# Performance work log

Hardware: AMD Instinct MI355X
Metric: run time of the kernel (lower is better)

Reference implementation:

```python
import jax, jax.numpy as jnp
import numpy as np

HEADS = 8
DIM_HEAD = 64
DIM = 512
EPS = 1e-7  # module's self.eps, also used as LayerNorm eps


def _per_head_layernorm(t, w, b):
    # t: [b, h, n, d]; w, b: [h, d] (one LayerNorm per head, affine)
    mu = t.mean(axis=-1, keepdims=True)
    var = t.var(axis=-1, keepdims=True)  # biased, matches torch LayerNorm
    tn = (t - mu) * jax.lax.rsqrt(var + EPS)
    return tn * w[None, :, None, :] + b[None, :, None, :]


def setup_inputs() -> dict:
    key = jax.random.key(0)
    ks = jax.random.split(key, 4)
    inner = HEADS * DIM_HEAD
    return {
        "x": jax.random.normal(ks[0], (2, 2048, DIM), dtype=jnp.float32),
        "w_qkv": jax.random.normal(ks[1], (3 * inner, DIM), dtype=jnp.float32) * 0.02,
        "lnk_w": jnp.ones((HEADS, DIM_HEAD), dtype=jnp.float32),
        "lnk_b": jnp.zeros((HEADS, DIM_HEAD), dtype=jnp.float32),
        "lnv_w": jnp.ones((HEADS, DIM_HEAD), dtype=jnp.float32),
        "lnv_b": jnp.zeros((HEADS, DIM_HEAD), dtype=jnp.float32),
        "w_out": jax.random.normal(ks[2], (DIM, inner), dtype=jnp.float32) * 0.02,
        "b_out": jnp.zeros((DIM,), dtype=jnp.float32),
    }


def reference(x, w_qkv, lnk_w, lnk_b, lnv_w, lnv_b, w_out, b_out):
    b, n, _ = x.shape
    qkv = x @ w_qkv.T  # [b, n, 3*inner]
    q, k, v = jnp.split(qkv, 3, axis=-1)

    def split_heads(t):  # [b, n, h*d] -> [b, h, n, d]
        return t.reshape(b, n, HEADS, DIM_HEAD).transpose(0, 2, 1, 3)

    q, k, v = map(split_heads, (q, k, v))

    # per-head LayerNorm over dim_head on k and v
    k = _per_head_layernorm(k, lnk_w, lnk_b)
    v = _per_head_layernorm(v, lnv_w, lnv_b)

    # causal linear attention: prefix sums of k and of k-v outer products
    k_cum = jnp.cumsum(k, axis=2)  # [b, h, n, d]
    # scores: [b, h, n, d, e] prefix sums of outer products, scaled by 1/seq_len
    scores = jnp.cumsum(jnp.einsum('bhnd,bhne->bhnde', k, v), axis=2) / n
    d_inv = 1.0 / jnp.einsum('bhnd,bhnd->bhn', k_cum + EPS, q)  # [b, h, n]
    out = jnp.einsum('bhnd,bhnde,bhn->bhne', q, scores, d_inv)  # [b, h, n, e]

    out = out.transpose(0, 2, 1, 3).reshape(b, n, HEADS * DIM_HEAD)  # b n (h e)
    return out @ w_out.T + b_out
```

## Files before the change

### kernel.cpp

```cpp
#include <hip/hip_runtime.h>

constexpr int Bb   = 2;
constexpr int Nn   = 2048;
constexpr int Hh   = 8;
constexpr int Dd   = 64;
constexpr int Mm   = Bb * Nn;
constexpr int TQKV = 1536;
constexpr int INNER = Hh * Dd;
constexpr int CH   = 64;
constexpr int NCH  = Nn / CH;
constexpr int CSZ  = Dd * Dd + Dd;
constexpr float EPSF = 1e-7f;

typedef _Float16 half8 __attribute__((ext_vector_type(8)));
typedef _Float16 half4 __attribute__((ext_vector_type(4)));
typedef float f32x4 __attribute__((ext_vector_type(4)));

#define AS1(p) ((const __attribute__((address_space(1))) unsigned int*)(p))
#define AS3(p) ((__attribute__((address_space(3))) unsigned int*)(p))

__global__ __launch_bounds__(256) void gemm1_f32(
    const float* __restrict__ A, const float* __restrict__ B,
    float* __restrict__ C,
    const float* __restrict__ lnk_w, const float* __restrict__ lnk_b) {
  __shared__ float pool[8704];
  __shared__ float mean_s[128], inv_s[128];
  float* As = pool;
  float* Bs = pool + 4224;
  const int tid = threadIdx.x;
  const int tx = tid & 15, ty = tid >> 4;
  const int bm = blockIdx.y * 128, bn = blockIdx.x * 64;
  const int rowA = tid & 127, c4a = tid >> 7;
  const int rowB = tid & 63,  c4b = tid >> 6;

  float acc[8][4] = {};

  for (int k0 = 0; k0 < 512; k0 += 32) {
#pragma unroll
    for (int p = 0; p < 4; ++p) {
      int c4 = c4a + 2 * p;
      float4 fa = *(const float4*)(A + (size_t)(bm + rowA) * 512 + k0 + c4 * 4);
      As[(c4 * 4 + 0) * 132 + rowA] = fa.x; As[(c4 * 4 + 1) * 132 + rowA] = fa.y;
      As[(c4 * 4 + 2) * 132 + rowA] = fa.z; As[(c4 * 4 + 3) * 132 + rowA] = fa.w;
    }
#pragma unroll
    for (int p = 0; p < 2; ++p) {
      int c4 = c4b + 4 * p;
      float4 fb = *(const float4*)(B + (size_t)(bn + rowB) * 512 + k0 + c4 * 4);
      Bs[(c4 * 4 + 0) * 68 + rowB] = fb.x; Bs[(c4 * 4 + 1) * 68 + rowB] = fb.y;
      Bs[(c4 * 4 + 2) * 68 + rowB] = fb.z; Bs[(c4 * 4 + 3) * 68 + rowB] = fb.w;
    }
    __syncthreads();
#pragma unroll
    for (int kk = 0; kk < 32; ++kk) {
      float a[8], b[4];
      *(float4*)&a[0] = *(const float4*)&As[kk * 132 + ty * 8];
      *(float4*)&a[4] = *(const float4*)&As[kk * 132 + ty * 8 + 4];
      *(float4*)&b[0] = *(const float4*)&Bs[kk * 68 + tx * 4];
#pragma unroll
      for (int i = 0; i < 8; ++i)
#pragma unroll
        for (int j = 0; j < 4; ++j) acc[i][j] += a[i] * b[j];
    }
    __syncthreads();
  }

  if (bn < 512) {
#pragma unroll
    for (int i = 0; i < 8; ++i) {
      size_t row = bm + ty * 8 + i;
      float4 r;
      r.x = acc[i][0]; r.y = acc[i][1]; r.z = acc[i][2]; r.w = acc[i][3];
      *(float4*)(C + row * (size_t)TQKV + bn + tx * 4) = r;
    }
  } else {
#pragma unroll
    for (int i = 0; i < 8; ++i)
#pragma unroll
      for (int j = 0; j < 4; ++j)
        pool[(ty * 8 + i) * 68 + tx * 4 + j] = acc[i][j];
    __syncthreads();
    if (tid < 128) {
      const float* R = pool + tid * 68;
      float s = 0.f, s2 = 0.f;
#pragma unroll
      for (int j = 0; j < 64; j += 4) {
        float4 v = *(const float4*)&R[j];
        s += v.x + v.y + v.z + v.w;
        s2 += v.x * v.x + v.y * v.y + v.z * v.z + v.w * v.w;
      }
      float mean = s * (1.f / 64.f);
      float var = s2 * (1.f / 64.f) - mean * mean;
      mean_s[tid] = mean;
      inv_s[tid] = 1.0f / sqrtf(var + EPSF);
    }
    __syncthreads();
    const int h = (bn - 512) >> 6;
    for (int i = tid; i < 128 * 16; i += 256) {
      int row = i >> 4, c4 = i & 15;
      float4 v = *(const float4*)&pool[row * 68 + c4 * 4];
      float4 w = *(const float4*)(lnk_w + h * 64 + c4 * 4);
      float4 bb = *(const float4*)(lnk_b + h * 64 + c4 * 4);
      float m = mean_s[row], iv = inv_s[row];
      float4 r;
      r.x = (v.x - m) * iv * w.x + bb.x;
      r.y = (v.y - m) * iv * w.y + bb.y;
      r.z = (v.z - m) * iv * w.z + bb.z;
      r.w = (v.w - m) * iv * w.w + bb.w;
      *(float4*)(C + (size_t)(bm + row) * TQKV + bn + c4 * 4) = r;
    }
  }
}

__global__ __launch_bounds__(256) void split_f16_k(
    const float* __restrict__ s, _Float16* __restrict__ hi,
    _Float16* __restrict__ lo, int n4) {
  int i = blockIdx.x * 256 + threadIdx.x;
  if (i >= n4) return;
  float4 a = ((const float4*)s)[i];
  half4 h, l;
  float av[4] = {a.x, a.y, a.z, a.w};
#pragma unroll
  for (int j = 0; j < 4; ++j) {
    _Float16 hh = (_Float16)av[j];
    h[j] = hh;
    l[j] = (_Float16)((av[j] - (float)hh) * 2048.0f);
  }
  ((half4*)hi)[i] = h;
  ((half4*)lo)[i] = l;
}

__global__ __launch_bounds__(256) void gemm_split_nt(
    const _Float16* __restrict__ Ah, const _Float16* __restrict__ Al,
    const _Float16* __restrict__ Bh, const _Float16* __restrict__ Bl,
    const float* __restrict__ bias, float* __restrict__ C,
    int Ndim, int Kd,
    const float* __restrict__ lnw, const float* __restrict__ lnb) {
  constexpr int BM = 128, BN = 64, BK = 32;
  __shared__ float pool[8704];
  __shared__ float mean_s[128], inv_s[128];
  _Float16* lds = (_Float16*)pool;
  constexpr int AHo = 0;
  constexpr int ALo = BM * BK;
  constexpr int BHo = 2 * BM * BK;
  constexpr int BLo = 2 * BM * BK + BN * BK;

  const int tid = threadIdx.x;
  const int wave = tid >> 6, lane = tid & 63;
  const int lq = lane >> 4, lm = lane & 15;
  const int bm = blockIdx.y * BM, bn = blockIdx.x * BN;

  f32x4 acc[2][4] = {};
  f32x4 corr[2][4] = {};

  const int nsteps = Kd >> 5;
  for (int ks = 0; ks < nsteps; ++ks) {
    const int k0 = ks * BK;
    for (int idx = wave; idx < 24; idx += 4) {
      int t, j;
      if (idx < 8)       { t = 0; j = idx; }
      else if (idx < 16) { t = 1; j = idx - 8; }
      else if (idx < 20) { t = 2; j = idx - 16; }
      else               { t = 3; j = idx - 20; }
      const int row = j * 16 + (lane >> 2);
      const _Float16* g;
      _Float16* l;
      if (t == 0)      { g = Ah + (size_t)(bm + row) * Kd; l = lds + AHo + j * 16 * BK; }
      else if (t == 1) { g = Al + (size_t)(bm + row) * Kd; l = lds + ALo + j * 16 * BK; }
      else if (t == 2) { g = Bh + (size_t)(bn + row) * Kd; l = lds + BHo + j * 16 * BK; }
      else             { g = Bl + (size_t)(bn + row) * Kd; l = lds + BLo + j * 16 * BK; }
      g += k0 + (lane & 3) * 8;
      __builtin_amdgcn_global_load_lds(AS1(g), AS3(l), 16, 0, 0);
    }
    __syncthreads();

    half8 ahf[2], alf[2], bhf[4], blf[4];
    const int mwo = wave * 32;
#pragma unroll
    for (int fi = 0; fi < 2; ++fi) {
      ahf[fi] = *(const half8*)&lds[AHo + (mwo + fi * 16 + lm) * BK + lq * 8];
      alf[fi] = *(const half8*)&lds[ALo + (mwo + fi * 16 + lm) * BK + lq * 8];
    }
#pragma unroll
    for (int fj = 0; fj < 4; ++fj) {
      bhf[fj] = *(const half8*)&lds[BHo + (fj * 16 + lm) * BK + lq * 8];
      blf[fj] = *(const half8*)&lds[BLo + (fj * 16 + lm) * BK + lq * 8];
    }
#pragma unroll
    for (int fi = 0; fi < 2; ++fi)
#pragma unroll
      for (int fj = 0; fj < 4; ++fj) {
        acc[fi][fj] = __builtin_amdgcn_mfma_f32_16x16x32_f16(
            ahf[fi], bhf[fj], acc[fi][fj], 0, 0, 0);
        corr[fi][fj] = __builtin_amdgcn_mfma_f32_16x16x32_f16(
            ahf[fi], blf[fj], corr[fi][fj], 0, 0, 0);
        corr[fi][fj] = __builtin_amdgcn_mfma_f32_16x16x32_f16(
            alf[fi], bhf[fj], corr[fi][fj], 0, 0, 0);
      }
    __syncthreads();
  }

  if (!lnw) {
#pragma unroll
    for (int fi = 0; fi < 2; ++fi) {
      const int m0 = bm + wave * 32 + fi * 16 + lq * 4;
#pragma unroll
      for (int fj = 0; fj < 4; ++fj) {
        const int n = bn + fj * 16 + lm;
        const float bb = bias ? bias[n] : 0.f;
        f32x4 v = acc[fi][fj];
        f32x4 cv = corr[fi][fj];
#pragma unroll
        for (int r = 0; r < 4; ++r)
          C[(size_t)(m0 + r) * Ndim + n] = v[r] + cv[r] * (1.0f / 2048.0f) + bb;
      }
    }
  } else {
#pragma unroll
    for (int fi = 0; fi < 2; ++fi) {
      const int r0 = wave * 32 + fi * 16 + lq * 4;
#pragma unroll
      for (int fj = 0; fj < 4; ++fj) {
        const int n = fj * 16 + lm;
        f32x4 v = acc[fi][fj];
        f32x4 cv = corr[fi][fj];
#pragma unroll
        for (int r = 0; r < 4; ++r)
          pool[(r0 + r) * 68 + n] = v[r] + cv[r] * (1.0f / 2048.0f);
      }
    }
    __syncthreads();
    if (tid < 128) {
      const float* R = pool + tid * 68;
      float s = 0.f, s2 = 0.f;
#pragma unroll
      for (int j = 0; j < 64; j += 4) {
        float4 v = *(const float4*)&R[j];
        s += v.x + v.y + v.z + v.w;
        s2 += v.x * v.x + v.y * v.y + v.z * v.z + v.w * v.w;
      }
      float mean = s * (1.f / 64.f);
      float var = s2 * (1.f / 64.f) - mean * mean;
      mean_s[tid] = mean;
      inv_s[tid] = 1.0f / sqrtf(var + EPSF);
    }
    __syncthreads();
    const int h = bn >> 6;
    for (int i = tid; i < 128 * 16; i += 256) {
      int row = i >> 4, c4 = i & 15;
      float4 v = *(const float4*)&pool[row * 68 + c4 * 4];
      float4 w = *(const float4*)(lnw + h * 64 + c4 * 4);
      float4 bb = *(const float4*)(lnb + h * 64 + c4 * 4);
      float m = mean_s[row], iv = inv_s[row];
      float4 r;
      r.x = (v.x - m) * iv * w.x + bb.x;
      r.y = (v.y - m) * iv * w.y + bb.y;
      r.z = (v.z - m) * iv * w.z + bb.z;
      r.w = (v.w - m) * iv * w.w + bb.w;
      *(float4*)(C + (size_t)(bm + row) * Ndim + bn + c4 * 4) = r;
    }
  }
}

__global__ __launch_bounds__(256) void chunk_sums(
    const float* __restrict__ qkv, float* __restrict__ cbuf) {
  int blk = blockIdx.x;
  int c = blk % NCH;
  int bh = blk / NCH;
  int h = bh % Hh, b = bh / Hh;
  __shared__ float Ks[CH][68];
  __shared__ float Vs[CH][68];
  int tid = threadIdx.x;
  const float* base = qkv + (size_t)(b * Nn + c * CH) * TQKV + h * Dd;
  for (int i = tid; i < CH * 16; i += 256) {
    int row = i >> 4, c4 = i & 15;
    *(float4*)&Ks[row][c4 * 4] =
        *(const float4*)(base + (size_t)row * TQKV + INNER + c4 * 4);
    *(float4*)&Vs[row][c4 * 4] =
        *(const float4*)(base + (size_t)row * TQKV + 2 * INNER + c4 * 4);
  }
  __syncthreads();
  int d0 = (tid >> 4) * 4, e0 = (tid & 15) * 4;
  float acc[4][4] = {};
  float kc[4] = {0.f, 0.f, 0.f, 0.f};
  for (int n = 0; n < CH; ++n) {
    float4 kv = *(const float4*)&Ks[n][d0];
    float4 vv = *(const float4*)&Vs[n][e0];
    float ka[4] = {kv.x, kv.y, kv.z, kv.w};
    float va[4] = {vv.x, vv.y, vv.z, vv.w};
#pragma unroll
    for (int i = 0; i < 4; ++i)
#pragma unroll
      for (int j = 0; j < 4; ++j) acc[i][j] += ka[i] * va[j];
    if (e0 == 0) {
#pragma unroll
      for (int i = 0; i < 4; ++i) kc[i] += ka[i];
    }
  }
  float* out = cbuf + (size_t)blk * CSZ;
#pragma unroll
  for (int i = 0; i < 4; ++i) {
    float4 r;
    r.x = acc[i][0]; r.y = acc[i][1]; r.z = acc[i][2]; r.w = acc[i][3];
    *(float4*)(out + (size_t)(d0 + i) * Dd + e0) = r;
  }
  if (e0 == 0) {
#pragma unroll
    for (int i = 0; i < 4; ++i) out[Dd * Dd + d0 + i] = kc[i];
  }
}

__global__ __launch_bounds__(256) void chunk_prefix(float* __restrict__ cbuf) {
  int bh = blockIdx.y;
  int i = blockIdx.x * 256 + threadIdx.x;
  if (i >= CSZ) return;
  float* p = cbuf + (size_t)bh * NCH * CSZ + i;
  float carry = 0.f;
  for (int c = 0; c < NCH; ++c) {
    float t = p[(size_t)c * CSZ];
    p[(size_t)c * CSZ] = carry;
    carry += t;
  }
}

__global__ __launch_bounds__(256) void chunk_attn(
    const float* __restrict__ qkv, const float* __restrict__ cbuf,
    _Float16* __restrict__ atth, _Float16* __restrict__ attl) {
  int blk = blockIdx.x;
  int c = blk % NCH;
  int bh = blk / NCH;
  int h = bh % Hh, b = bh / Hh;
  __shared__ float Qs[64][68];
  __shared__ float Ks[64][68];
  __shared__ float Vs[64][68];
  __shared__ float Ss[64][68];
  __shared__ float kcs[64];
  __shared__ float rs[64][17];
  __shared__ float denomS[64];
  float (*Ps)[68] = Ks;

  int tid = threadIdx.x;
  int tx = tid & 15, ty = tid >> 4;
  const float* base = qkv + (size_t)(b * Nn + c * CH) * TQKV + h * Dd;
  for (int i = tid; i < CH * 16; i += 256) {
    int row = i >> 4, c4 = i & 15;
    float4 fq = *(const float4*)(base + (size_t)row * TQKV + c4 * 4);
    Qs[c4 * 4 + 0][row] = fq.x; Qs[c4 * 4 + 1][row] = fq.y;
    Qs[c4 * 4 + 2][row] = fq.z; Qs[c4 * 4 + 3][row] = fq.w;
    float4 fk = *(const float4*)(base + (size_t)row * TQKV + INNER + c4 * 4);
    Ks[c4 * 4 + 0][row] = fk.x; Ks[c4 * 4 + 1][row] = fk.y;
    Ks[c4 * 4 + 2][row] = fk.z; Ks[c4 * 4 + 3][row] = fk.w;
    float4 fv = *(const float4*)(base + (size_t)row * TQKV + 2 * INNER + c4 * 4);
    *(float4*)&Vs[row][c4 * 4] = fv;
  }
  const float* sp = cbuf + (size_t)blk * CSZ;
  for (int i = tid; i < 1024; i += 256) {
    int row = i >> 4;
    *(float4*)&Ss[row][(i & 15) * 4] = *(const float4*)(sp + (size_t)i * 4);
  }
  if (tid < 16) {
    float4 f = *(const float4*)(sp + Dd * Dd + tid * 4);
    kcs[tid * 4 + 0] = f.x; kcs[tid * 4 + 1] = f.y;
    kcs[tid * 4 + 2] = f.z; kcs[tid * 4 + 3] = f.w;
  }
  __syncthreads();

  float accP[4][4] = {};
  for (int kk = 0; kk < 64; ++kk) {
    float4 qa = *(const float4*)&Qs[kk][ty * 4];
    float4 kb = *(const float4*)&Ks[kk][tx * 4];
    float qv[4] = {qa.x, qa.y, qa.z, qa.w};
    float kv[4] = {kb.x, kb.y, kb.z, kb.w};
#pragma unroll
    for (int i = 0; i < 4; ++i)
#pragma unroll
      for (int j = 0; j < 4; ++j) accP[i][j] += qv[i] * kv[j];
  }
  __syncthreads();

#pragma unroll
  for (int i = 0; i < 4; ++i) {
    int n = ty * 4 + i;
    float rsum = 0.f;
#pragma unroll
    for (int j = 0; j < 4; ++j) {
      int m = tx * 4 + j;
      float p = (m <= n) ? accP[i][j] : 0.f;
      Ps[m][n] = p;
      rsum += p;
    }
    rs[n][tx] = rsum;
  }
  __syncthreads();

  float accO[4][4] = {};
  for (int d = 0; d < 64; ++d) {
    float4 qa = *(const float4*)&Qs[d][ty * 4];
    float4 sb = *(const float4*)&Ss[d][tx * 4];
    float qv[4] = {qa.x, qa.y, qa.z, qa.w};
    float sv[4] = {sb.x, sb.y, sb.z, sb.w};
#pragma unroll
    for (int i = 0; i < 4; ++i)
#pragma unroll
      for (int j = 0; j < 4; ++j) accO[i][j] += qv[i] * sv[j];
  }
  if (tid < 64) {
    int n = tid;
    float qkc = 0.f, qs = 0.f;
    for (int d = 0; d < 64; ++d) {
      float q = Qs[d][n];
      qkc += q * kcs[d];
      qs += q;
    }
    float rsum = 0.f;
#pragma unroll
    for (int t2 = 0; t2 < 16; ++t2) rsum += rs[n][t2];
    denomS[n] = qkc + rsum + EPSF * qs;
  }
  __syncthreads();

  for (int m = 0; m < 64; ++m) {
    float4 pa = *(const float4*)&Ps[m][ty * 4];
    float4 vb = *(const float4*)&Vs[m][tx * 4];
    float pv[4] = {pa.x, pa.y, pa.z, pa.w};
    float vv[4] = {vb.x, vb.y, vb.z, vb.w};
#pragma unroll
    for (int i = 0; i < 4; ++i)
#pragma unroll
      for (int j = 0; j < 4; ++j) accO[i][j] += pv[i] * vv[j];
  }

  size_t obase = (size_t)(b * Nn + c * CH) * INNER + h * Dd;
#pragma unroll
  for (int i = 0; i < 4; ++i) {
    int n = ty * 4 + i;
    float dinv = 1.0f / denomS[n];
    float scale = dinv * (1.0f / (float)Nn);
    half4 hv, lv;
#pragma unroll
    for (int j = 0; j < 4; ++j) {
      float o = accO[i][j] * scale;
      _Float16 hh = (_Float16)o;
      hv[j] = hh;
      lv[j] = (_Float16)((o - (float)hh) * 2048.0f);
    }
    *(half4*)(atth + obase + (size_t)n * INNER + tx * 4) = hv;
    *(half4*)(attl + obase + (size_t)n * INNER + tx * 4) = lv;
  }
}

extern "C" void kernel_launch(void* const* d_in, const int* in_sizes, int n_in,
                              void* d_out, int out_size, void* d_ws,
                              size_t ws_size, hipStream_t stream) {
  const float* x     = (const float*)d_in[0];
  const float* w_qkv = (const float*)d_in[1];
  const float* lnk_w = (const float*)d_in[2];
  const float* lnk_b = (const float*)d_in[3];
  const float* lnv_w = (const float*)d_in[4];
  const float* lnv_b = (const float*)d_in[5];
  const float* w_out = (const float*)d_in[6];
  const float* b_out = (const float*)d_in[7];
  float* out = (float*)d_out;

  float* qkv  = (float*)d_ws;
  float* cbuf = qkv + (size_t)Mm * TQKV;
  _Float16* atth = (_Float16*)(cbuf + (size_t)Bb * Hh * NCH * CSZ);
  _Float16* attl = atth + (size_t)Mm * INNER;
  _Float16* woh  = attl + (size_t)Mm * INNER;
  _Float16* wol  = woh + (size_t)INNER * 512;
  _Float16* xh   = wol + (size_t)INNER * 512;
  _Float16* xl   = xh + (size_t)Mm * 512;
  _Float16* wvh  = xl + (size_t)Mm * 512;
  _Float16* wvl  = wvh + (size_t)INNER * 512;

  split_f16_k<<<2048, 256, 0, stream>>>(x, xh, xl, Mm * 512 / 4);
  split_f16_k<<<256, 256, 0, stream>>>(
      w_qkv + (size_t)1024 * 512, wvh, wvl, INNER * 512 / 4);

  gemm1_f32<<<dim3(1024 / 64, Mm / 128), 256, 0, stream>>>(
      x, w_qkv, qkv, lnk_w, lnk_b);

  gemm_split_nt<<<dim3(512 / 64, Mm / 128), 256, 0, stream>>>(
      xh, xl, wvh, wvl, nullptr, qkv + 1024, TQKV, 512, lnv_w, lnv_b);

  chunk_sums<<<Bb * Hh * NCH, 256, 0, stream>>>(qkv, cbuf);

  chunk_prefix<<<dim3((CSZ + 255) / 256, Bb * Hh), 256, 0, stream>>>(cbuf);

  split_f16_k<<<256, 256, 0, stream>>>(w_out, woh, wol, INNER * 512 / 4);

  chunk_attn<<<Bb * Hh * NCH, 256, 0, stream>>>(qkv, cbuf, atth, attl);

  gemm_split_nt<<<dim3(INNER / 64, Mm / 128), 256, 0, stream>>>(
      atth, attl, woh, wol, b_out, out, INNER, 512, nullptr, nullptr);
}
```

Before: 236.0 us.

## Merge split kernels and QKV GEMMs into batched launches; fuse attention loops

Combines the three fp16 hi/lo split launches into one batched kernel. It also merges the fp32 Q/K GEMM and the split-fp16 V GEMM into one grid that dispatches on block index, so the V-projection blocks run alongside the Q/K blocks. In chunk_attn, the Q·K and Q·S accumulation loops become one pass that shares the Q loads. The aim is fewer kernel launches and better GPU fill, at the cost of a heterogeneous grid and more register pressure in the fused attention loop.

```diff
diff --git a/kernel.cpp b/kernel.cpp
--- a/kernel.cpp
+++ b/kernel.cpp
@@ -19,66 +19,119 @@
 #define AS1(p) ((const __attribute__((address_space(1))) unsigned int*)(p))
 #define AS3(p) ((__attribute__((address_space(3))) unsigned int*)(p))
 
-__global__ __launch_bounds__(256) void gemm1_f32(
+__global__ __launch_bounds__(256) void split_batched(
+    const float* __restrict__ x, _Float16* __restrict__ xh,
+    _Float16* __restrict__ xl,
+    const float* __restrict__ wv, _Float16* __restrict__ wvh,
+    _Float16* __restrict__ wvl,
+    const float* __restrict__ wo, _Float16* __restrict__ woh,
+    _Float16* __restrict__ wol) {
+  int bid = blockIdx.x;
+  const float* s;
+  _Float16 *hi, *lo;
+  int i;
+  if (bid < 2048)      { s = x;  hi = xh;  lo = xl;  i = bid * 256 + threadIdx.x; }
+  else if (bid < 2304) { s = wv; hi = wvh; lo = wvl; i = (bid - 2048) * 256 + threadIdx.x; }
+  else                 { s = wo; hi = woh; lo = wol; i = (bid - 2304) * 256 + threadIdx.x; }
+  float4 a = ((const float4*)s)[i];
+  half4 h, l;
+  float av[4] = {a.x, a.y, a.z, a.w};
+#pragma unroll
+  for (int j = 0; j < 4; ++j) {
+    _Float16 hh = (_Float16)av[j];
+    h[j] = hh;
+    l[j] = (_Float16)((av[j] - (float)hh) * 2048.0f);
+  }
+  ((half4*)hi)[i] = h;
+  ((half4*)lo)[i] = l;
+}
+
+__global__ __launch_bounds__(256) void mega_gemm1(
     const float* __restrict__ A, const float* __restrict__ B,
-    float* __restrict__ C,
-    const float* __restrict__ lnk_w, const float* __restrict__ lnk_b) {
+    float* __restrict__ qkv,
+    const float* __restrict__ lnk_w, const float* __restrict__ lnk_b,
+    const _Float16* __restrict__ xh, const _Float16* __restrict__ xl,
+    const _Float16* __restrict__ wvh, const _Float16* __restrict__ wvl,
+    const float* __restrict__ lnv_w, const float* __restrict__ lnv_b) {
   __shared__ float pool[8704];
   __shared__ float mean_s[128], inv_s[128];
-  float* As = pool;
-  float* Bs = pool + 4224;
   const int tid = threadIdx.x;
-  const int tx = tid & 15, ty = tid >> 4;
-  const int bm = blockIdx.y * 128, bn = blockIdx.x * 64;
-  const int rowA = tid & 127, c4a = tid >> 7;
-  const int rowB = tid & 63,  c4b = tid >> 6;
-
-  float acc[8][4] = {};
-
-  for (int k0 = 0; k0 < 512; k0 += 32) {
-#pragma unroll
-    for (int p = 0; p < 4; ++p) {
-      int c4 = c4a + 2 * p;
-      float4 fa = *(const float4*)(A + (size_t)(bm + rowA) * 512 + k0 + c4 * 4);
-      As[(c4 * 4 + 0) * 132 + rowA] = fa.x; As[(c4 * 4 + 1) * 132 + rowA] = fa.y;
-      As[(c4 * 4 + 2) * 132 + rowA] = fa.z; As[(c4 * 4 + 3) * 132 + rowA] = fa.w;
-    }
-#pragma unroll
-    for (int p = 0; p < 2; ++p) {
-      int c4 = c4b + 4 * p;
-      float4 fb = *(const float4*)(B + (size_t)(bn + rowB) * 512 + k0 + c4 * 4);
-      Bs[(c4 * 4 + 0) * 68 + rowB] = fb.x; Bs[(c4 * 4 + 1) * 68 + rowB] = fb.y;
-      Bs[(c4 * 4 + 2) * 68 + rowB] = fb.z; Bs[(c4 * 4 + 3) * 68 + rowB] = fb.w;
-    }
-    __syncthreads();
-#pragma unroll
-    for (int kk = 0; kk < 32; ++kk) {
-      float a[8], b[4];
-      *(float4*)&a[0] = *(const float4*)&As[kk * 132 + ty * 8];
-      *(float4*)&a[4] = *(const float4*)&As[kk * 132 + ty * 8 + 4];
-      *(float4*)&b[0] = *(const float4*)&Bs[kk * 68 + tx * 4];
-#pragma unroll
-      for (int i = 0; i < 8; ++i)
-#pragma unroll
-        for (int j = 0; j < 4; ++j) acc[i][j] += a[i] * b[j];
-    }
-    __syncthreads();
-  }
-
-  if (bn < 512) {
-#pragma unroll
-    for (int i = 0; i < 8; ++i) {
-      size_t row = bm + ty * 8 + i;
-      float4 r;
-      r.x = acc[i][0]; r.y = acc[i][1]; r.z = acc[i][2]; r.w = acc[i][3];
-      *(float4*)(C + row * (size_t)TQKV + bn + tx * 4) = r;
-    }
-  } else {
-#pragma unroll
-    for (int i = 0; i < 8; ++i)
-#pragma unroll
-      for (int j = 0; j < 4; ++j)
-        pool[(ty * 8 + i) * 68 + tx * 4 + j] = acc[i][j];
+  const int bid = blockIdx.x;
+
+  if (bid < 256) {
+    constexpr int BM = 128, BN = 64, BK = 32;
+    _Float16* lds = (_Float16*)pool;
+    constexpr int AHo = 0;
+    constexpr int ALo = BM * BK;
+    constexpr int BHo = 2 * BM * BK;
+    constexpr int BLo = 2 * BM * BK + BN * BK;
+    const int wave = tid >> 6, lane = tid & 63;
+    const int lq = lane >> 4, lm = lane & 15;
+    const int bm = (bid >> 3) * BM, bn = (bid & 7) * BN;
+    float* C = qkv + 1024;
+
+    f32x4 acc[2][4] = {};
+    f32x4 corr[2][4] = {};
+
+    for (int ks = 0; ks < 16; ++ks) {
+      const int k0 = ks * BK;
+      for (int idx = wave; idx < 24; idx += 4) {
+        int t, j;
+        if (idx < 8)       { t = 0; j = idx; }
+        else if (idx < 16) { t = 1; j = idx - 8; }
+        else if (idx < 20) { t = 2; j = idx - 16; }
+        else               { t = 3; j = idx - 20; }
+        const int row = j * 16 + (lane >> 2);
+        const _Float16* g;
+        _Float16* l;
+        if (t == 0)      { g = xh + (size_t)(bm + row) * 512; l = lds + AHo + j * 16 * BK; }
+        else if (t == 1) { g = xl + (size_t)(bm + row) * 512; l = lds + ALo + j * 16 * BK; }
+        else if (t == 2) { g = wvh + (size_t)(bn + row) * 512; l = lds + BHo + j * 16 * BK; }
+        else             { g = wvl + (size_t)(bn + row) * 512; l = lds + BLo + j * 16 * BK; }
+        g += k0 + (lane & 3) * 8;
+        __builtin_amdgcn_global_load_lds(AS1(g), AS3(l), 16, 0, 0);
+      }
+      __syncthreads();
+
+      half8 ahf[2], alf[2], bhf[4], blf[4];
+      const int mwo = wave * 32;
+#pragma unroll
+      for (int fi = 0; fi < 2; ++fi) {
+        ahf[fi] = *(const half8*)&lds[AHo + (mwo + fi * 16 + lm) * BK + lq * 8];
+        alf[fi] = *(const half8*)&lds[ALo + (mwo + fi * 16 + lm) * BK + lq * 8];
+      }
+#pragma unroll
+      for (int fj = 0; fj < 4; ++fj) {
+        bhf[fj] = *(const half8*)&lds[BHo + (fj * 16 + lm) * BK + lq * 8];
+        blf[fj] = *(const half8*)&lds[BLo + (fj * 16 + lm) * BK + lq * 8];
+      }
+#pragma unroll
+      for (int fi = 0; fi < 2; ++fi)
+#pragma unroll
+        for (int fj = 0; fj < 4; ++fj) {
+          acc[fi][fj] = __builtin_amdgcn_mfma_f32_16x16x32_f16(
+              ahf[fi], bhf[fj], acc[fi][fj], 0, 0, 0);
+          corr[fi][fj] = __builtin_amdgcn_mfma_f32_16x16x32_f16(
+              ahf[fi], blf[fj], corr[fi][fj], 0, 0, 0);
+          corr[fi][fj] = __builtin_amdgcn_mfma_f32_16x16x32_f16(
+              alf[fi], bhf[fj], corr[fi][fj], 0, 0, 0);
+        }
+      __syncthreads();
+    }
+
+#pragma unroll
+    for (int fi = 0; fi < 2; ++fi) {
+      const int r0 = wave * 32 + fi * 16 + lq * 4;
+#pragma unroll
+      for (int fj = 0; fj < 4; ++fj) {
+        const int n = fj * 16 + lm;
+        f32x4 v = acc[fi][fj];
+        f32x4 cv = corr[fi][fj];
+#pragma unroll
+        for (int r = 0; r < 4; ++r)
+          pool[(r0 + r) * 68 + n] = v[r] + cv[r] * (1.0f / 2048.0f);
+      }
+    }
     __syncthreads();
     if (tid < 128) {
       const float* R = pool + tid * 68;
@@ -95,12 +148,12 @@
       inv_s[tid] = 1.0f / sqrtf(var + EPSF);
     }
     __syncthreads();
-    const int h = (bn - 512) >> 6;
+    const int h = bn >> 6;
     for (int i = tid; i < 128 * 16; i += 256) {
       int row = i >> 4, c4 = i & 15;
       float4 v = *(const float4*)&pool[row * 68 + c4 * 4];
-      float4 w = *(const float4*)(lnk_w + h * 64 + c4 * 4);
-      float4 bb = *(const float4*)(lnk_b + h * 64 + c4 * 4);
+      float4 w = *(const float4*)(lnv_w + h * 64 + c4 * 4);
+      float4 bb = *(const float4*)(lnv_b + h * 64 + c4 * 4);
       float m = mean_s[row], iv = inv_s[row];
       float4 r;
       r.x = (v.x - m) * iv * w.x + bb.x;
@@ -109,37 +162,105 @@
       r.w = (v.w - m) * iv * w.w + bb.w;
       *(float4*)(C + (size_t)(bm + row) * TQKV + bn + c4 * 4) = r;
     }
-  }
-}
-
-__global__ __launch_bounds__(256) void split_f16_k(
-    const float* __restrict__ s, _Float16* __restrict__ hi,
-    _Float16* __restrict__ lo, int n4) {
-  int i = blockIdx.x * 256 + threadIdx.x;
-  if (i >= n4) return;
-  float4 a = ((const float4*)s)[i];
-  half4 h, l;
-  float av[4] = {a.x, a.y, a.z, a.w};
-#pragma unroll
-  for (int j = 0; j < 4; ++j) {
-    _Float16 hh = (_Float16)av[j];
-    h[j] = hh;
-    l[j] = (_Float16)((av[j] - (float)hh) * 2048.0f);
-  }
-  ((half4*)hi)[i] = h;
-  ((half4*)lo)[i] = l;
+    return;
+  }
+
+  {
+    const int fb = bid - 256;
+    const int tx = tid & 15, ty = tid >> 4;
+    const int bm = (fb >> 4) * 128, bn = (fb & 15) * 64;
+    float* As = pool;
+    float* Bs = pool + 4224;
+    const int rowA = tid & 127, c4a = tid >> 7;
+    const int rowB = tid & 63,  c4b = tid >> 6;
+
+    float acc[8][4] = {};
+
+    for (int k0 = 0; k0 < 512; k0 += 32) {
+#pragma unroll
+      for (int p = 0; p < 4; ++p) {
+        int c4 = c4a + 2 * p;
+        float4 fa = *(const float4*)(A + (size_t)(bm + rowA) * 512 + k0 + c4 * 4);
+        As[(c4 * 4 + 0) * 132 + rowA] = fa.x; As[(c4 * 4 + 1) * 132 + rowA] = fa.y;
+        As[(c4 * 4 + 2) * 132 + rowA] = fa.z; As[(c4 * 4 + 3) * 132 + rowA] = fa.w;
+      }
+#pragma unroll
+      for (int p = 0; p < 2; ++p) {
+        int c4 = c4b + 4 * p;
+        float4 fb4 = *(const float4*)(B + (size_t)(bn + rowB) * 512 + k0 + c4 * 4);
+        Bs[(c4 * 4 + 0) * 68 + rowB] = fb4.x; Bs[(c4 * 4 + 1) * 68 + rowB] = fb4.y;
+        Bs[(c4 * 4 + 2) * 68 + rowB] = fb4.z; Bs[(c4 * 4 + 3) * 68 + rowB] = fb4.w;
+      }
+      __syncthreads();
+#pragma unroll
+      for (int kk = 0; kk < 32; ++kk) {
+        float a[8], b[4];
+        *(float4*)&a[0] = *(const float4*)&As[kk * 132 + ty * 8];
+        *(float4*)&a[4] = *(const float4*)&As[kk * 132 + ty * 8 + 4];
+        *(float4*)&b[0] = *(const float4*)&Bs[kk * 68 + tx * 4];
+#pragma unroll
+        for (int i = 0; i < 8; ++i)
+#pragma unroll
+          for (int j = 0; j < 4; ++j) acc[i][j] += a[i] * b[j];
+      }
+      __syncthreads();
+    }
+
+    if (bn < 512) {
+#pragma unroll
+      for (int i = 0; i < 8; ++i) {
+        size_t row = bm + ty * 8 + i;
+        float4 r;
+        r.x = acc[i][0]; r.y = acc[i][1]; r.z = acc[i][2]; r.w = acc[i][3];
+        *(float4*)(qkv + row * (size_t)TQKV + bn + tx * 4) = r;
+      }
+    } else {
+#pragma unroll
+      for (int i = 0; i < 8; ++i)
+#pragma unroll
+        for (int j = 0; j < 4; ++j)
+          pool[(ty * 8 + i) * 68 + tx * 4 + j] = acc[i][j];
+      __syncthreads();
+      if (tid < 128) {
+        const float* R = pool + tid * 68;
+        float s = 0.f, s2 = 0.f;
+#pragma unroll
+        for (int j = 0; j < 64; j += 4) {
+          float4 v = *(const float4*)&R[j];
+          s += v.x + v.y + v.z + v.w;
+          s2 += v.x * v.x + v.y * v.y + v.z * v.z + v.w * v.w;
+        }
+        float mean = s * (1.f / 64.f);
+        float var = s2 * (1.f / 64.f) - mean * mean;
+        mean_s[tid] = mean;
+        inv_s[tid] = 1.0f / sqrtf(var + EPSF);
+      }
+      __syncthreads();
+      const int h = (bn - 512) >> 6;
+      for (int i = tid; i < 128 * 16; i += 256) {
+        int row = i >> 4, c4 = i & 15;
+        float4 v = *(const float4*)&pool[row * 68 + c4 * 4];
+        float4 w = *(const float4*)(lnk_w + h * 64 + c4 * 4);
+        float4 bb = *(const float4*)(lnk_b + h * 64 + c4 * 4);
+        float m = mean_s[row], iv = inv_s[row];
+        float4 r;
+        r.x = (v.x - m) * iv * w.x + bb.x;
+        r.y = (v.y - m) * iv * w.y + bb.y;
+        r.z = (v.z - m) * iv * w.z + bb.z;
+        r.w = (v.w - m) * iv * w.w + bb.w;
+        *(float4*)(qkv + (size_t)(bm + row) * TQKV + bn + c4 * 4) = r;
+      }
+    }
+  }
 }
 
 __global__ __launch_bounds__(256) void gemm_split_nt(
     const _Float16* __restrict__ Ah, const _Float16* __restrict__ Al,
     const _Float16* __restrict__ Bh, const _Float16* __restrict__ Bl,
     const float* __restrict__ bias, float* __restrict__ C,
-    int Ndim, int Kd,
-    const float* __restrict__ lnw, const float* __restrict__ lnb) {
+    int Ndim, int Kd) {
   constexpr int BM = 128, BN = 64, BK = 32;
-  __shared__ float pool[8704];
-  __shared__ float mean_s[128], inv_s[128];
-  _Float16* lds = (_Float16*)pool;
+  __shared__ _Float16 lds[(2 * BM + 2 * BN) * BK];
   constexpr int AHo = 0;
   constexpr int ALo = BM * BK;
   constexpr int BHo = 2 * BM * BK;
@@ -200,64 +321,18 @@
     __syncthreads();
   }
 
-  if (!lnw) {
-#pragma unroll
-    for (int fi = 0; fi < 2; ++fi) {
-      const int m0 = bm + wave * 32 + fi * 16 + lq * 4;
-#pragma unroll
-      for (int fj = 0; fj < 4; ++fj) {
-        const int n = bn + fj * 16 + lm;
-        const float bb = bias ? bias[n] : 0.f;
-        f32x4 v = acc[fi][fj];
-        f32x4 cv = corr[fi][fj];
-#pragma unroll
-        for (int r = 0; r < 4; ++r)
-          C[(size_t)(m0 + r) * Ndim + n] = v[r] + cv[r] * (1.0f / 2048.0f) + bb;
-      }
-    }
-  } else {
-#pragma unroll
-    for (int fi = 0; fi < 2; ++fi) {
-      const int r0 = wave * 32 + fi * 16 + lq * 4;
-#pragma unroll
-      for (int fj = 0; fj < 4; ++fj) {
-        const int n = fj * 16 + lm;
-        f32x4 v = acc[fi][fj];
-        f32x4 cv = corr[fi][fj];
-#pragma unroll
-        for (int r = 0; r < 4; ++r)
-          pool[(r0 + r) * 68 + n] = v[r] + cv[r] * (1.0f / 2048.0f);
-      }
-    }
-    __syncthreads();
-    if (tid < 128) {
-      const float* R = pool + tid * 68;
-      float s = 0.f, s2 = 0.f;
-#pragma unroll
-      for (int j = 0; j < 64; j += 4) {
-        float4 v = *(const float4*)&R[j];
-        s += v.x + v.y + v.z + v.w;
-        s2 += v.x * v.x + v.y * v.y + v.z * v.z + v.w * v.w;
-      }
-      float mean = s * (1.f / 64.f);
-      float var = s2 * (1.f / 64.f) - mean * mean;
-      mean_s[tid] = mean;
-      inv_s[tid] = 1.0f / sqrtf(var + EPSF);
-    }
-    __syncthreads();
-    const int h = bn >> 6;
-    for (int i = tid; i < 128 * 16; i += 256) {
-      int row = i >> 4, c4 = i & 15;
-      float4 v = *(const float4*)&pool[row * 68 + c4 * 4];
-      float4 w = *(const float4*)(lnw + h * 64 + c4 * 4);
-      float4 bb = *(const float4*)(lnb + h * 64 + c4 * 4);
-      float m = mean_s[row], iv = inv_s[row];
-      float4 r;
-      r.x = (v.x - m) * iv * w.x + bb.x;
-      r.y = (v.y - m) * iv * w.y + bb.y;
-      r.z = (v.z - m) * iv * w.z + bb.z;
-      r.w = (v.w - m) * iv * w.w + bb.w;
-      *(float4*)(C + (size_t)(bm + row) * Ndim + bn + c4 * 4) = r;
+#pragma unroll
+  for (int fi = 0; fi < 2; ++fi) {
+    const int m0 = bm + wave * 32 + fi * 16 + lq * 4;
+#pragma unroll
+    for (int fj = 0; fj < 4; ++fj) {
+      const int n = bn + fj * 16 + lm;
+      const float bb = bias ? bias[n] : 0.f;
+      f32x4 v = acc[fi][fj];
+      f32x4 cv = corr[fi][fj];
+#pragma unroll
+      for (int r = 0; r < 4; ++r)
+        C[(size_t)(m0 + r) * Ndim + n] = v[r] + cv[r] * (1.0f / 2048.0f) + bb;
     }
   }
 }
@@ -366,15 +441,21 @@
   __syncthreads();
 
   float accP[4][4] = {};
+  float accO[4][4] = {};
   for (int kk = 0; kk < 64; ++kk) {
     float4 qa = *(const float4*)&Qs[kk][ty * 4];
     float4 kb = *(const float4*)&Ks[kk][tx * 4];
+    float4 sb = *(const float4*)&Ss[kk][tx * 4];
     float qv[4] = {qa.x, qa.y, qa.z, qa.w};
     float kv[4] = {kb.x, kb.y, kb.z, kb.w};
+    float sv[4] = {sb.x, sb.y, sb.z, sb.w};
 #pragma unroll
     for (int i = 0; i < 4; ++i)
 #pragma unroll
-      for (int j = 0; j < 4; ++j) accP[i][j] += qv[i] * kv[j];
+      for (int j = 0; j < 4; ++j) {
+        accP[i][j] += qv[i] * kv[j];
+        accO[i][j] += qv[i] * sv[j];
+      }
   }
   __syncthreads();
 
@@ -393,17 +474,6 @@
   }
   __syncthreads();
 
-  float accO[4][4] = {};
-  for (int d = 0; d < 64; ++d) {
-    float4 qa = *(const float4*)&Qs[d][ty * 4];
-    float4 sb = *(const float4*)&Ss[d][tx * 4];
-    float qv[4] = {qa.x, qa.y, qa.z, qa.w};
-    float sv[4] = {sb.x, sb.y, sb.z, sb.w};
-#pragma unroll
-    for (int i = 0; i < 4; ++i)
-#pragma unroll
-      for (int j = 0; j < 4; ++j) accO[i][j] += qv[i] * sv[j];
-  }
   if (tid < 64) {
     int n = tid;
     float qkc = 0.f, qs = 0.f;
@@ -473,24 +543,18 @@
   _Float16* wvh  = xl + (size_t)Mm * 512;
   _Float16* wvl  = wvh + (size_t)INNER * 512;
 
-  split_f16_k<<<2048, 256, 0, stream>>>(x, xh, xl, Mm * 512 / 4);
-  split_f16_k<<<256, 256, 0, stream>>>(
-      w_qkv + (size_t)1024 * 512, wvh, wvl, INNER * 512 / 4);
-
-  gemm1_f32<<<dim3(1024 / 64, Mm / 128), 256, 0, stream>>>(
-      x, w_qkv, qkv, lnk_w, lnk_b);
-
-  gemm_split_nt<<<dim3(512 / 64, Mm / 128), 256, 0, stream>>>(
-      xh, xl, wvh, wvl, nullptr, qkv + 1024, TQKV, 512, lnv_w, lnv_b);
+  split_batched<<<2560, 256, 0, stream>>>(
+      x, xh, xl, w_qkv + (size_t)1024 * 512, wvh, wvl, w_out, woh, wol);
+
+  mega_gemm1<<<768, 256, 0, stream>>>(
+      x, w_qkv, qkv, lnk_w, lnk_b, xh, xl, wvh, wvl, lnv_w, lnv_b);
 
   chunk_sums<<<Bb * Hh * NCH, 256, 0, stream>>>(qkv, cbuf);
 
   chunk_prefix<<<dim3((CSZ + 255) / 256, Bb * Hh), 256, 0, stream>>>(cbuf);
 
-  split_f16_k<<<256, 256, 0, stream>>>(w_out, woh, wol, INNER * 512 / 4);
-
   chunk_attn<<<Bb * Hh * NCH, 256, 0, stream>>>(qkv, cbuf, atth, attl);
 
   gemm_split_nt<<<dim3(INNER / 64, Mm / 128), 256, 0, stream>>>(
-      atth, attl, woh, wol, b_out, out, INNER, 512, nullptr, nullptr);
-}
+      atth, attl, woh, wol, b_out, out, INNER, 512);
+}
```

After: 258.6 us. 9.6% more time.
